# Kernel tuning notes

Measured on AMD Instinct MI355X. Metric: run time of the kernel, lower is better.

Reference implementation:

```python
import jax, jax.numpy as jnp
import numpy as np

B, S, D = 1, 2048, 1024
H, KD = 16, 64          # heads, key_dim = hidden/heads
VD, HS = 2048, 128      # v_dim = 2*hidden (double_v_dim), head_size = v_dim/heads
EPS = 1e-5


def rotate_every_two(x):
    x1 = x[..., ::2]
    x2 = x[..., 1::2]
    return jnp.stack((-x2, x1), axis=-1).reshape(x.shape)


def setup_inputs() -> dict:
    key = jax.random.key(0)
    ks = jax.random.split(key, 8)
    x = jax.random.normal(ks[0], (B, S, D), jnp.float32)
    # rotary-style sin/cos, shape [S, KD]
    pos = jnp.arange(S, dtype=jnp.float32)
    inv_freq = 1.0 / (10000.0 ** (jnp.arange(0, KD, 2, dtype=jnp.float32) / KD))
    ang = jnp.repeat(pos[:, None] * inv_freq[None, :], 2, axis=-1)  # [S, KD]
    sin, cos = jnp.sin(ang), jnp.cos(ang)
    # RetNet per-head decay mask, shape [H, S, S]
    gammas = 1.0 - 2.0 ** (-5.0 - jnp.arange(H, dtype=jnp.float32))
    n = jnp.arange(S, dtype=jnp.float32)
    diff = n[:, None] - n[None, :]                    # [S, S]
    mask = jnp.where(diff >= 0, gammas[:, None, None] ** diff[None, :, :], 0.0)
    mask = mask / jnp.sqrt(jnp.sum(mask, axis=-1, keepdims=True))
    # projection weights stored [in, out] (equivalent to torch Linear W^T)
    gain = 2.0 ** (-2.5)
    Wq = gain * jax.random.normal(ks[1], (D, D), jnp.float32) * (2.0 / (D + D)) ** 0.5
    Wk = gain * jax.random.normal(ks[2], (D, D), jnp.float32) * (2.0 / (D + D)) ** 0.5
    Wv = gain * jax.random.normal(ks[3], (D, VD), jnp.float32) * (2.0 / (D + VD)) ** 0.5
    Wg = gain * jax.random.normal(ks[4], (D, VD), jnp.float32) * (2.0 / (D + VD)) ** 0.5
    Wo = jax.random.normal(ks[5], (VD, D), jnp.float32) * (2.0 / (VD + D)) ** 0.5
    gn_w = jnp.ones((VD,), jnp.float32)
    gn_b = jnp.zeros((VD,), jnp.float32)
    return {"x": x, "sin": sin, "cos": cos, "mask": mask,
            "Wq": Wq, "Wk": Wk, "Wv": Wv, "Wg": Wg, "Wo": Wo,
            "gn_w": gn_w, "gn_b": gn_b}


def reference(x, sin, cos, mask, Wq, Wk, Wv, Wg, Wo, gn_w, gn_b):
    scaling = KD ** (-0.5)
    q = (x @ Wq).reshape(B, S, H, KD).transpose(0, 2, 1, 3)            # [B,H,S,KD]
    k = ((x @ Wk) * scaling).reshape(B, S, H, KD).transpose(0, 2, 1, 3)
    v = x @ Wv                                                          # [B,S,VD]
    g = x @ Wg
    qr = q * cos + rotate_every_two(q) * sin                            # theta_shift
    kr = k * cos + rotate_every_two(k) * sin
    vr = v.reshape(B, S, H, HS).transpose(0, 2, 1, 3)                   # [B,H,S,HS]
    qk = jnp.einsum('bhsd,bhtd->bhst', qr, kr) * mask                  # [B,H,S,S]
    den = jnp.clip(jnp.abs(jax.lax.stop_gradient(qk).sum(-1, keepdims=True)), 1.0, None)
    o = jnp.einsum('bhst,bhtv->bhsv', qk / den, vr)                    # [B,H,S,HS]
    o = o.transpose(0, 2, 1, 3).reshape(S, H * HS)                      # bsz==1 reshape
    # GroupNorm(H groups over VD channels), rows are the batch dim
    og = o.reshape(S, H, HS)
    mu = og.mean(-1, keepdims=True)
    var = og.var(-1, keepdims=True)
    og = (og - mu) * jax.lax.rsqrt(var + EPS)
    o = (og * gn_w.reshape(H, HS) + gn_b.reshape(H, HS)).reshape(B, S, VD)
    out = (g * jax.nn.sigmoid(g)) * o                                   # swish gate
    return out @ Wo                                                     # [B,S,D]
```

## Files before the change

### kernel.cpp

```cpp
#include <hip/hip_runtime.h>
#include <cstdint>
#include <cstddef>

typedef unsigned short u16;
typedef u16   u16x8 __attribute__((ext_vector_type(8)));
typedef u16   u16x4 __attribute__((ext_vector_type(4)));
typedef u16   u16x2 __attribute__((ext_vector_type(2)));
typedef float f32x4 __attribute__((ext_vector_type(4)));

#define S_LEN 2048

static __device__ __forceinline__ u16 f2bf(float f){
  union { float f; unsigned u; } v; v.f = f;
  unsigned r = (v.u + 0x7FFFu + ((v.u >> 16) & 1u)) >> 16;
  return (u16)r;
}
static __device__ __forceinline__ float bf2f(u16 u){
  union { unsigned u; float f; } v; v.u = ((unsigned)u) << 16; return v.f;
}

static __device__ __forceinline__ void mfma16(f32x4& c, u16x8 a, u16x8 b){
  asm("s_nop 1\n\tv_mfma_f32_16x16x32_bf16 %0, %1, %2, %0"
      : "+v"(c) : "v"(a), "v"(b));
}

#if defined(__has_builtin)
#  if __has_builtin(__builtin_amdgcn_global_load_lds)
#    define USE_GLDS 1
#  endif
#endif

static __device__ __forceinline__ void stage16(const u16* g, u16* l){
#ifdef USE_GLDS
  __builtin_amdgcn_global_load_lds((const __attribute__((address_space(1))) void*)g,
                                   (__attribute__((address_space(3))) void*)l,
                                   16, 0, 0);
#else
  *(u16x8*)l = *(const u16x8*)g;
#endif
}

__global__ __launch_bounds__(256) void cvt_x_kernel(const float* __restrict__ x,
                                                    u16* __restrict__ xb){
  int i = (blockIdx.x * 256 + threadIdx.x) * 4;
  float4 v = *(const float4*)(x + i);
  u16x4 o; o[0] = f2bf(v.x); o[1] = f2bf(v.y); o[2] = f2bf(v.z); o[3] = f2bf(v.w);
  *(u16x4*)(xb + i) = o;
}

__global__ __launch_bounds__(256) void transpose_all(
    const float* __restrict__ Wq, const float* __restrict__ Wk,
    const float* __restrict__ Wv, const float* __restrict__ Wg,
    const float* __restrict__ Wo, u16* __restrict__ WT, u16* __restrict__ WoT){
  __shared__ float tile[32][33];
  int bid = blockIdx.x;
  const float* W; u16* dst; int K, N, lb, lgx; float scale = 1.0f;
  if (bid < 1024)      { W=Wq; dst=WT;                        K=1024; N=1024; lb=bid;        lgx=5; }
  else if (bid < 2048) { W=Wk; dst=WT + (size_t)1024 * 1024;  K=1024; N=1024; lb=bid - 1024; lgx=5; scale=0.125f; }
  else if (bid < 4096) { W=Wv; dst=WT + (size_t)2048 * 1024;  K=1024; N=2048; lb=bid - 2048; lgx=6; }
  else if (bid < 6144) { W=Wg; dst=WT + (size_t)4096 * 1024;  K=1024; N=2048; lb=bid - 4096; lgx=6; }
  else                 { W=Wo; dst=WoT;                       K=2048; N=1024; lb=bid - 6144; lgx=5; }
  int n0 = (lb & ((1 << lgx) - 1)) * 32;
  int k0 = (lb >> lgx) * 32;
  int tx = threadIdx.x & 31, ty = threadIdx.x >> 5;
  #pragma unroll
  for (int i = 0; i < 32; i += 8)
    tile[ty + i][tx] = W[(size_t)(k0 + ty + i) * N + n0 + tx];
  __syncthreads();
  #pragma unroll
  for (int i = 0; i < 32; i += 8)
    dst[(size_t)(n0 + ty + i) * K + k0 + tx] = f2bf(scale * tile[tx][ty + i]);
}

template<int MODE, int BN>
__global__ __launch_bounds__(256) void gemm2(
    const u16* __restrict__ A, const u16* __restrict__ BT, int K,
    float* __restrict__ outF,
    u16* __restrict__ oq, u16* __restrict__ ok,
    u16* __restrict__ ovT, u16* __restrict__ og,
    const float* __restrict__ sinb, const float* __restrict__ cosb)
{
  constexpr int NI = BN / 32;
  constexpr int LB_LOADS = BN * 8 / 256;
  constexpr int TL = 4 + LB_LOADS;

  __shared__ u16 lA[2][128 * 64];
  __shared__ u16 lB[2][BN * 64];

  const int t = threadIdx.x;
  const int lane = t & 63, w = t >> 6;
  const int r = lane & 15, g4 = lane >> 4;
  const int bm = blockIdx.y * 128, bn = blockIdx.x * BN;
  const int wm = (w & 1) * 64, wn = (w >> 1) * (BN / 2);

  f32x4 acc[4][NI] = {};

  auto STAGE = [&](int buf, int kb){
    #pragma unroll
    for (int p = 0; p < 4; ++p){
      int ci = p * 256 + t;
      int row = ci >> 3, ch = ci & 7;
      stage16(A + (size_t)(bm + row) * K + kb + ((ch ^ (row & 7)) * 8),
              &lA[buf][ci * 8]);
    }
    #pragma unroll
    for (int p = 0; p < LB_LOADS; ++p){
      int ci = p * 256 + t;
      int row = ci >> 3, ch = ci & 7;
      stage16(BT + (size_t)(bn + row) * K + kb + ((ch ^ (row & 7)) * 8),
              &lB[buf][ci * 8]);
    }
  };

  STAGE(0, 0);
  int cur = 0;
  for (int kb = 0; kb < K; kb += 64){
    if (kb + 64 < K){
      STAGE(cur ^ 1, kb + 64);
      if constexpr (TL == 8) asm volatile("s_waitcnt vmcnt(8)" ::: "memory");
      else                   asm volatile("s_waitcnt vmcnt(6)" ::: "memory");
    } else {
      asm volatile("s_waitcnt vmcnt(0)" ::: "memory");
    }
    __builtin_amdgcn_s_barrier();

    #pragma unroll
    for (int j = 0; j < 2; ++j){
      u16x8 af[4], bfr[NI];
      #pragma unroll
      for (int i = 0; i < 4; ++i){
        int row = wm + 16 * i + r;
        af[i] = *(const u16x8*)&lA[cur][row * 64 + (((j * 4 + g4) ^ (row & 7)) * 8)];
      }
      #pragma unroll
      for (int i = 0; i < NI; ++i){
        int row = wn + 16 * i + r;
        bfr[i] = *(const u16x8*)&lB[cur][row * 64 + (((j * 4 + g4) ^ (row & 7)) * 8)];
      }
      #pragma unroll
      for (int mi = 0; mi < 4; ++mi)
        #pragma unroll
        for (int ni = 0; ni < NI; ++ni)
          mfma16(acc[mi][ni], af[mi], bfr[ni]);
    }
    asm volatile("s_waitcnt lgkmcnt(0)" ::: "memory");
    __builtin_amdgcn_s_barrier();
    cur ^= 1;
  }

  if constexpr (MODE == 2){
    #pragma unroll
    for (int mi = 0; mi < 4; ++mi)
      #pragma unroll
      for (int ni = 0; ni < NI; ++ni)
        #pragma unroll
        for (int rr = 0; rr < 4; ++rr){
          int row = bm + wm + 16 * mi + 4 * g4 + rr;
          int col = bn + wn + 16 * ni + r;
          outF[(size_t)row * 1024 + col] = acc[mi][ni][rr];
        }
  } else {
    if (bn < 2048){
      #pragma unroll
      for (int mi = 0; mi < 4; ++mi)
        #pragma unroll
        for (int ni = 0; ni < NI; ++ni){
          int n = bn + wn + 16 * ni + r;
          int kd = n & 63;
          #pragma unroll
          for (int rr = 0; rr < 4; ++rr){
            int srow = bm + wm + 16 * mi + 4 * g4 + rr;
            float v = acc[mi][ni][rr];
            float pv = __shfl_xor(v, 1);
            float cs = cosb[srow * 64 + kd];
            float sn = sinb[srow * 64 + kd];
            float o = v * cs + ((n & 1) ? pv : -pv) * sn;
            u16 ob = f2bf(o);
            if (n < 1024) oq[((size_t)(n >> 6)          * S_LEN + srow) * 64 + kd] = ob;
            else          ok[((size_t)((n - 1024) >> 6) * S_LEN + srow) * 64 + kd] = ob;
          }
        }
    } else if (bn < 4096){
      #pragma unroll
      for (int mi = 0; mi < 4; ++mi)
        #pragma unroll
        for (int ni = 0; ni < NI; ++ni){
          int n = (bn - 2048) + wn + 16 * ni + r;
          int srow0 = bm + wm + 16 * mi + 4 * g4;
          u16x4 pk;
          #pragma unroll
          for (int rr = 0; rr < 4; ++rr) pk[rr] = f2bf(acc[mi][ni][rr]);
          *(u16x4*)&ovT[(size_t)n * S_LEN + srow0] = pk;
        }
    } else {
      #pragma unroll
      for (int mi = 0; mi < 4; ++mi)
        #pragma unroll
        for (int ni = 0; ni < NI; ++ni){
          int n = (bn - 4096) + wn + 16 * ni + r;
          int srow0 = bm + wm + 16 * mi + 4 * g4;
          #pragma unroll
          for (int rr = 0; rr < 4; ++rr)
            og[(size_t)(srow0 + rr) * 2048 + n] = f2bf(acc[mi][ni][rr]);
        }
    }
  }
}

__global__ __launch_bounds__(256) void retention2(const u16* __restrict__ qrb,
                                                  const u16* __restrict__ krb,
                                                  const u16* __restrict__ vTb,
                                                  float* __restrict__ obuf){
  __shared__ u16 kt[2][64 * 64];
  __shared__ u16 vt[2][128 * 64];
  __shared__ u16 pb[4][16 * 88];

  const int idx = blockIdx.x;
  const int h  = idx & 15;
  const int sb = (idx < 256) ? (31 - (idx >> 4)) : ((idx >> 4) - 16);
  const int s0 = sb * 64;
  const int t  = threadIdx.x;
  const int w  = t >> 6, lane = t & 63;
  const int r  = lane & 15, g4 = lane >> 4;
  const int s0w = s0 + 16 * w;

  const float om   = exp2f(-5.0f - (float)h);
  const float lg   = logf(1.0f - om);
  const float l2g  = lg * 1.44269504088896f;
  const float dmax = 30.0f / (-l2g);

  int t0 = 0;
  {
    float tf = (float)(s0 - 63) - dmax;
    if (tf > 0.0f) t0 = ((int)tf) & ~63;
  }

  const u16* qrow = qrb + ((size_t)h * S_LEN + (s0w + r)) * 64 + 8 * g4;
  u16x8 qf0 = *(const u16x8*)(qrow);
  u16x8 qf1 = *(const u16x8*)(qrow + 32);

  float invn[4];
  #pragma unroll
  for (int rr = 0; rr < 4; ++rr){
    int s = s0w + 4 * g4 + rr;
    invn[rr] = rsqrtf(-expm1f((float)(s + 1) * lg) / om);
  }
  float bsub[4];
  {
    float e_r  = exp2f(-(float)r * l2g);
    float e16  = exp2f(-16.0f * l2g);
    bsub[0] = e_r; bsub[1] = bsub[0] * e16; bsub[2] = bsub[1] * e16; bsub[3] = bsub[2] * e16;
  }

  f32x4 oacc[8] = {};
  float rs[4] = {0.f, 0.f, 0.f, 0.f};

  auto STAGE = [&](int buf, int tb){
    #pragma unroll
    for (int p = 0; p < 2; ++p){
      int ci = p * 256 + t;
      int row = ci >> 3, ch = ci & 7;
      const u16* src = krb + ((size_t)h * S_LEN + tb + row) * 64 + ((ch ^ (row & 7)) * 8);
      stage16(src, &kt[buf][ci * 8]);
    }
    #pragma unroll
    for (int p = 0; p < 4; ++p){
      int ci = p * 256 + t;
      int row = ci >> 3, ch = ci & 7;
      const u16* src = vTb + ((size_t)(h * 128 + row)) * S_LEN + tb + ((ch ^ (row & 7)) * 8);
      stage16(src, &vt[buf][ci * 8]);
    }
  };

  STAGE(0, t0);
  int cur = 0;
  for (int tb = t0; tb <= s0; tb += 64){
    const bool last = (tb + 64 > s0);
    if (!last){
      STAGE(cur ^ 1, tb + 64);
      asm volatile("s_waitcnt vmcnt(6)" ::: "memory");
    } else {
      asm volatile("s_waitcnt vmcnt(0)" ::: "memory");
    }
    __builtin_amdgcn_s_barrier();

    if (tb <= s0w + 15 && (float)(s0w - tb - 63) <= dmax){
      f32x4 p[4] = {};
      #pragma unroll
      for (int sub = 0; sub < 4; ++sub){
        int row = 16 * sub + r;
        u16x8 kf0 = *(const u16x8*)&kt[cur][row * 64 + ((g4       ^ (row & 7)) * 8)];
        u16x8 kf1 = *(const u16x8*)&kt[cur][row * 64 + (((4 + g4) ^ (row & 7)) * 8)];
        mfma16(p[sub], qf0, kf0);
        mfma16(p[sub], qf1, kf1);
      }
      asm volatile("s_nop 7\n\ts_nop 7"
                   : "+v"(p[0]), "+v"(p[1]), "+v"(p[2]), "+v"(p[3]));
      float arr[4];
      #pragma unroll
      for (int rr = 0; rr < 4; ++rr)
        arr[rr] = exp2f((float)(s0w + 4 * g4 + rr - tb) * l2g) * invn[rr];
      #pragma unroll
      for (int sub = 0; sub < 4; ++sub){
        int tt = tb + 16 * sub + r;
        #pragma unroll
        for (int rr = 0; rr < 4; ++rr){
          int srow = s0w + 4 * g4 + rr;
          float dec = (srow >= tt) ? arr[rr] * bsub[sub] : 0.0f;
          float val = p[sub][rr] * dec;
          rs[rr] += val;
          pb[w][(4 * g4 + rr) * 88 + 16 * sub + r] = f2bf(val);
        }
      }
      asm volatile("s_waitcnt lgkmcnt(0)" ::: "memory");
      __builtin_amdgcn_sched_barrier(0);
      u16x8 pf0 = *(const u16x8*)&pb[w][r * 88 + 8 * g4];
      u16x8 pf1 = *(const u16x8*)&pb[w][r * 88 + 32 + 8 * g4];
      #pragma unroll
      for (int cs = 0; cs < 8; ++cs){
        int row = 16 * cs + r;
        u16x8 vf0 = *(const u16x8*)&vt[cur][row * 64 + ((g4       ^ (row & 7)) * 8)];
        u16x8 vf1 = *(const u16x8*)&vt[cur][row * 64 + (((4 + g4) ^ (row & 7)) * 8)];
        mfma16(oacc[cs], pf0, vf0);
        mfma16(oacc[cs], pf1, vf1);
      }
    }
    asm volatile("s_waitcnt lgkmcnt(0)" ::: "memory");
    __builtin_amdgcn_s_barrier();
    cur ^= 1;
  }

  #pragma unroll
  for (int rr = 0; rr < 4; ++rr){
    float v = rs[rr];
    v += __shfl_xor(v, 1); v += __shfl_xor(v, 2);
    v += __shfl_xor(v, 4); v += __shfl_xor(v, 8);
    float den = fabsf(v); if (den < 1.0f) den = 1.0f;
    rs[rr] = 1.0f / den;
  }
  #pragma unroll
  for (int cs = 0; cs < 8; ++cs)
    #pragma unroll
    for (int rr = 0; rr < 4; ++rr){
      int s = s0w + 4 * g4 + rr;
      obuf[((size_t)h * S_LEN + s) * 128 + 16 * cs + r] = oacc[cs][rr] * rs[rr];
    }
}

__global__ __launch_bounds__(256) void gn_gate_kernel(const float* __restrict__ obuf,
                                                      const u16* __restrict__ gb,
                                                      const float* __restrict__ gnw,
                                                      const float* __restrict__ gnb,
                                                      u16* __restrict__ gated){
  int s = blockIdx.x;
  int w = threadIdx.x >> 6, lane = threadIdx.x & 63;
  for (int h = w; h < 16; h += 4){
    const float* op = obuf + ((size_t)h * S_LEN + s) * 128 + lane * 2;
    float v0 = op[0], v1 = op[1];
    float sum = v0 + v1;
    #pragma unroll
    for (int m = 1; m < 64; m <<= 1) sum += __shfl_xor(sum, m);
    float mu = sum * (1.0f / 128.0f);
    float d0 = v0 - mu, d1 = v1 - mu;
    float sq = d0 * d0 + d1 * d1;
    #pragma unroll
    for (int m = 1; m < 64; m <<= 1) sq += __shfl_xor(sq, m);
    float rstd = rsqrtf(sq * (1.0f / 128.0f) + 1e-5f);
    int c = h * 128 + lane * 2;
    float n0 = d0 * rstd * gnw[c]     + gnb[c];
    float n1 = d1 * rstd * gnw[c + 1] + gnb[c + 1];
    u16x2 gv = *(const u16x2*)(gb + (size_t)s * 2048 + c);
    float g0 = bf2f(gv[0]), g1 = bf2f(gv[1]);
    float r0 = g0 / (1.0f + __expf(-g0)) * n0;
    float r1 = g1 / (1.0f + __expf(-g1)) * n1;
    u16x2 o2; o2[0] = f2bf(r0); o2[1] = f2bf(r1);
    *(u16x2*)(gated + (size_t)s * 2048 + c) = o2;
  }
}

extern "C" void kernel_launch(void* const* d_in, const int* in_sizes, int n_in,
                              void* d_out, int out_size, void* d_ws, size_t ws_size,
                              hipStream_t stream)
{
  (void)in_sizes; (void)n_in; (void)out_size; (void)ws_size;
  const float* x    = (const float*)d_in[0];
  const float* sinb = (const float*)d_in[1];
  const float* cosb = (const float*)d_in[2];
  const float* Wq   = (const float*)d_in[4];
  const float* Wk   = (const float*)d_in[5];
  const float* Wv   = (const float*)d_in[6];
  const float* Wg   = (const float*)d_in[7];
  const float* Wo   = (const float*)d_in[8];
  const float* gnw  = (const float*)d_in[9];
  const float* gnb  = (const float*)d_in[10];
  float* out = (float*)d_out;

  char* ws = (char*)d_ws;
  u16*   xb    = (u16*)  (ws + 0);
  u16*   WT    = (u16*)  (ws + ((size_t)4  << 20));
  float* obuf  = (float*)(ws + 0);
  u16*   WoT   = (u16*)  (ws + ((size_t)16 << 20));
  u16*   qrb   = (u16*)  (ws + ((size_t)20 << 20));
  u16*   krb   = (u16*)  (ws + ((size_t)24 << 20));
  u16*   gated = (u16*)  (ws + ((size_t)20 << 20));
  u16*   vTb   = (u16*)  (ws + ((size_t)28 << 20));
  u16*   gbuf  = (u16*)  (ws + ((size_t)36 << 20));

  cvt_x_kernel<<<dim3(2048), dim3(256), 0, stream>>>(x, xb);
  transpose_all<<<dim3(8192), dim3(256), 0, stream>>>(Wq, Wk, Wv, Wg, Wo, WT, WoT);

  gemm2<0, 128><<<dim3(48, 16), dim3(256), 0, stream>>>(xb, WT, 1024,
      nullptr, qrb, krb, vTb, gbuf, sinb, cosb);

  retention2<<<dim3(512), dim3(256), 0, stream>>>(qrb, krb, vTb, obuf);

  gn_gate_kernel<<<dim3(2048), dim3(256), 0, stream>>>(obuf, gbuf, gnw, gnb, gated);

  gemm2<2, 64><<<dim3(16, 16), dim3(256), 0, stream>>>(gated, WoT, 2048,
      out, nullptr, nullptr, nullptr, nullptr, nullptr, nullptr);
}
```

Before: 146.0 us.

## Fuse GroupNorm and swish gate into retention epilogue; merge prep kernels

```diff
diff --git a/kernel.cpp b/kernel.cpp
--- a/kernel.cpp
+++ b/kernel.cpp
@@ -40,20 +40,20 @@
 #endif
 }
 
-__global__ __launch_bounds__(256) void cvt_x_kernel(const float* __restrict__ x,
-                                                    u16* __restrict__ xb){
-  int i = (blockIdx.x * 256 + threadIdx.x) * 4;
-  float4 v = *(const float4*)(x + i);
-  u16x4 o; o[0] = f2bf(v.x); o[1] = f2bf(v.y); o[2] = f2bf(v.z); o[3] = f2bf(v.w);
-  *(u16x4*)(xb + i) = o;
-}
-
-__global__ __launch_bounds__(256) void transpose_all(
+__global__ __launch_bounds__(256) void prep_all(
+    const float* __restrict__ x, u16* __restrict__ xb,
     const float* __restrict__ Wq, const float* __restrict__ Wk,
     const float* __restrict__ Wv, const float* __restrict__ Wg,
     const float* __restrict__ Wo, u16* __restrict__ WT, u16* __restrict__ WoT){
   __shared__ float tile[32][33];
   int bid = blockIdx.x;
+  if (bid >= 8192){
+    int i = ((bid - 8192) * 256 + threadIdx.x) * 4;
+    float4 v = *(const float4*)(x + i);
+    u16x4 o; o[0] = f2bf(v.x); o[1] = f2bf(v.y); o[2] = f2bf(v.z); o[3] = f2bf(v.w);
+    *(u16x4*)(xb + i) = o;
+    return;
+  }
   const float* W; u16* dst; int K, N, lb, lgx; float scale = 1.0f;
   if (bid < 1024)      { W=Wq; dst=WT;                        K=1024; N=1024; lb=bid;        lgx=5; }
   else if (bid < 2048) { W=Wk; dst=WT + (size_t)1024 * 1024;  K=1024; N=1024; lb=bid - 1024; lgx=5; scale=0.125f; }
@@ -207,10 +207,13 @@
   }
 }
 
-__global__ __launch_bounds__(256) void retention2(const u16* __restrict__ qrb,
-                                                  const u16* __restrict__ krb,
-                                                  const u16* __restrict__ vTb,
-                                                  float* __restrict__ obuf){
+__global__ __launch_bounds__(256) void retention_gn(const u16* __restrict__ qrb,
+                                                    const u16* __restrict__ krb,
+                                                    const u16* __restrict__ vTb,
+                                                    const u16* __restrict__ gbuf,
+                                                    const float* __restrict__ gnw,
+                                                    const float* __restrict__ gnb,
+                                                    u16* __restrict__ gated){
   __shared__ u16 kt[2][64 * 64];
   __shared__ u16 vt[2][128 * 64];
   __shared__ u16 pb[4][16 * 88];
@@ -338,43 +341,37 @@
     float den = fabsf(v); if (den < 1.0f) den = 1.0f;
     rs[rr] = 1.0f / den;
   }
-  #pragma unroll
-  for (int cs = 0; cs < 8; ++cs)
-    #pragma unroll
-    for (int rr = 0; rr < 4; ++rr){
-      int s = s0w + 4 * g4 + rr;
-      obuf[((size_t)h * S_LEN + s) * 128 + 16 * cs + r] = oacc[cs][rr] * rs[rr];
-    }
-}
-
-__global__ __launch_bounds__(256) void gn_gate_kernel(const float* __restrict__ obuf,
-                                                      const u16* __restrict__ gb,
-                                                      const float* __restrict__ gnw,
-                                                      const float* __restrict__ gnb,
-                                                      u16* __restrict__ gated){
-  int s = blockIdx.x;
-  int w = threadIdx.x >> 6, lane = threadIdx.x & 63;
-  for (int h = w; h < 16; h += 4){
-    const float* op = obuf + ((size_t)h * S_LEN + s) * 128 + lane * 2;
-    float v0 = op[0], v1 = op[1];
-    float sum = v0 + v1;
-    #pragma unroll
-    for (int m = 1; m < 64; m <<= 1) sum += __shfl_xor(sum, m);
-    float mu = sum * (1.0f / 128.0f);
-    float d0 = v0 - mu, d1 = v1 - mu;
-    float sq = d0 * d0 + d1 * d1;
-    #pragma unroll
-    for (int m = 1; m < 64; m <<= 1) sq += __shfl_xor(sq, m);
+
+  float gw[8], gbv[8];
+  #pragma unroll
+  for (int cs = 0; cs < 8; ++cs){
+    int gc = h * 128 + 16 * cs + r;
+    gw[cs]  = gnw[gc];
+    gbv[cs] = gnb[gc];
+  }
+  #pragma unroll
+  for (int rr = 0; rr < 4; ++rr){
+    int s = s0w + 4 * g4 + rr;
+    float vv[8], m = 0.0f;
+    #pragma unroll
+    for (int cs = 0; cs < 8; ++cs){ vv[cs] = oacc[cs][rr] * rs[rr]; m += vv[cs]; }
+    m += __shfl_xor(m, 1); m += __shfl_xor(m, 2);
+    m += __shfl_xor(m, 4); m += __shfl_xor(m, 8);
+    float mu = m * (1.0f / 128.0f);
+    float sq = 0.0f;
+    #pragma unroll
+    for (int cs = 0; cs < 8; ++cs){ float d = vv[cs] - mu; sq += d * d; }
+    sq += __shfl_xor(sq, 1); sq += __shfl_xor(sq, 2);
+    sq += __shfl_xor(sq, 4); sq += __shfl_xor(sq, 8);
     float rstd = rsqrtf(sq * (1.0f / 128.0f) + 1e-5f);
-    int c = h * 128 + lane * 2;
-    float n0 = d0 * rstd * gnw[c]     + gnb[c];
-    float n1 = d1 * rstd * gnw[c + 1] + gnb[c + 1];
-    u16x2 gv = *(const u16x2*)(gb + (size_t)s * 2048 + c);
-    float g0 = bf2f(gv[0]), g1 = bf2f(gv[1]);
-    float r0 = g0 / (1.0f + __expf(-g0)) * n0;
-    float r1 = g1 / (1.0f + __expf(-g1)) * n1;
-    u16x2 o2; o2[0] = f2bf(r0); o2[1] = f2bf(r1);
-    *(u16x2*)(gated + (size_t)s * 2048 + c) = o2;
+    #pragma unroll
+    for (int cs = 0; cs < 8; ++cs){
+      int gc = h * 128 + 16 * cs + r;
+      float nv = (vv[cs] - mu) * rstd * gw[cs] + gbv[cs];
+      float gv = bf2f(gbuf[(size_t)s * 2048 + gc]);
+      float res = gv / (1.0f + __expf(-gv)) * nv;
+      gated[(size_t)s * 2048 + gc] = f2bf(res);
+    }
   }
 }
 
@@ -398,23 +395,19 @@
   char* ws = (char*)d_ws;
   u16*   xb    = (u16*)  (ws + 0);
   u16*   WT    = (u16*)  (ws + ((size_t)4  << 20));
-  float* obuf  = (float*)(ws + 0);
+  u16*   gated = (u16*)  (ws + 0);
   u16*   WoT   = (u16*)  (ws + ((size_t)16 << 20));
   u16*   qrb   = (u16*)  (ws + ((size_t)20 << 20));
   u16*   krb   = (u16*)  (ws + ((size_t)24 << 20));
-  u16*   gated = (u16*)  (ws + ((size_t)20 << 20));
   u16*   vTb   = (u16*)  (ws + ((size_t)28 << 20));
   u16*   gbuf  = (u16*)  (ws + ((size_t)36 << 20));
 
-  cvt_x_kernel<<<dim3(2048), dim3(256), 0, stream>>>(x, xb);
-  transpose_all<<<dim3(8192), dim3(256), 0, stream>>>(Wq, Wk, Wv, Wg, Wo, WT, WoT);
+  prep_all<<<dim3(10240), dim3(256), 0, stream>>>(x, xb, Wq, Wk, Wv, Wg, Wo, WT, WoT);
 
   gemm2<0, 128><<<dim3(48, 16), dim3(256), 0, stream>>>(xb, WT, 1024,
       nullptr, qrb, krb, vTb, gbuf, sinb, cosb);
 
-  retention2<<<dim3(512), dim3(256), 0, stream>>>(qrb, krb, vTb, obuf);
-
-  gn_gate_kernel<<<dim3(2048), dim3(256), 0, stream>>>(obuf, gbuf, gnw, gnb, gated);
+  retention_gn<<<dim3(512), dim3(256), 0, stream>>>(qrb, krb, vTb, gbuf, gnw, gnb, gated);
 
   gemm2<2, 64><<<dim3(16, 16), dim3(256), 0, stream>>>(gated, WoT, 2048,
       out, nullptr, nullptr, nullptr, nullptr, nullptr, nullptr);
```

After: 136.6 us. 1.07x faster.
